# Optimization experiments

Hardware: AMD Instinct MI355X
Metric: run time of the kernel (lower is better)

Reference implementation:

```python
import jax, jax.numpy as jnp
import numpy as np

B, T = 2048, 512
H1, H2, H3 = 100, 60, 30


def _glorot(key, shape, fan):
    bound = 1.0 / np.sqrt(fan)
    return jax.random.uniform(key, shape, jnp.float32, -bound, bound)


def setup_inputs() -> dict:
    key = jax.random.key(0)
    ks = jax.random.split(key, 17)
    inp = {"x": jax.random.normal(ks[0], (B, T, 2), jnp.float32)}
    # layer 1: input 2 -> hidden 100
    inp["W_ih1"] = _glorot(ks[1], (H1, 2), H1)
    inp["W_hh1"] = _glorot(ks[2], (H1, H1), H1)
    inp["b_ih1"] = _glorot(ks[3], (H1,), H1)
    inp["b_hh1"] = _glorot(ks[4], (H1,), H1)
    # layer 2: 100 -> 60
    inp["W_ih2"] = _glorot(ks[5], (H2, H1), H2)
    inp["W_hh2"] = _glorot(ks[6], (H2, H2), H2)
    inp["b_ih2"] = _glorot(ks[7], (H2,), H2)
    inp["b_hh2"] = _glorot(ks[8], (H2,), H2)
    # layer 3: 60 -> 30
    inp["W_ih3"] = _glorot(ks[9], (H3, H2), H3)
    inp["W_hh3"] = _glorot(ks[10], (H3, H3), H3)
    inp["b_ih3"] = _glorot(ks[11], (H3,), H3)
    inp["b_hh3"] = _glorot(ks[12], (H3,), H3)
    # heads
    inp["W_o1"] = _glorot(ks[13], (10, H3), 10)
    inp["b_o1"] = _glorot(ks[14], (10,), 10)
    inp["W_o2"] = _glorot(ks[15], (2, 10), 2)
    inp["b_o2"] = _glorot(ks[16], (2,), 2)
    return inp


def rnn_layer(x, W_ih, W_hh, b_ih, b_hh):
    # x: [B, T, in]; precompute the time-parallel input projection once
    xp = jnp.einsum("bti,hi->bth", x, W_ih) + (b_ih + b_hh)  # [B, T, H]
    h0 = jnp.zeros((x.shape[0], W_hh.shape[0]), x.dtype)

    def step(h, xt):  # xt: [B, H]
        h = jnp.tanh(xt + h @ W_hh.T)
        return h, h

    _, ys = jax.lax.scan(step, h0, jnp.swapaxes(xp, 0, 1))  # [T, B, H]
    return jnp.swapaxes(ys, 0, 1)  # [B, T, H]


def reference(x, W_ih1, W_hh1, b_ih1, b_hh1, W_ih2, W_hh2, b_ih2, b_hh2,
              W_ih3, W_hh3, b_ih3, b_hh3, W_o1, b_o1, W_o2, b_o2):
    h = rnn_layer(x, W_ih1, W_hh1, b_ih1, b_hh1)
    h = rnn_layer(h, W_ih2, W_hh2, b_ih2, b_hh2)
    h = rnn_layer(h, W_ih3, W_hh3, b_ih3, b_hh3)
    o = jnp.einsum("bth,oh->bto", h, W_o1) + b_o1
    return jnp.einsum("bto,po->btp", o, W_o2) + b_o2  # [B, T, 2]
```

## Files before the change

### kernel.cpp

```cpp
#include <hip/hip_runtime.h>

typedef _Float16 v8hf __attribute__((ext_vector_type(8)));
typedef float    v4f  __attribute__((ext_vector_type(4)));

#define MFMA16(a, b, c) __builtin_amdgcn_mfma_f32_16x16x32_f16((a), (b), (c), 0, 0, 0)

#define TT 512
#define BT 16
#define NTH 1024

#define PBLK  8192u
#define H2OFF 4352u
#define H3OFF 6656u
#define XSTO  16384u
#define RINGO 49152u

__shared__ __align__(64) char SM[57344];

__device__ __forceinline__ v4f tanh4(v4f r) {
    const float KS = 2.8853900817779268f;
    const float CL = 13.8498724f;
    float z0 = __builtin_amdgcn_fmed3f(r[0] * KS, -CL, CL);
    float z1 = __builtin_amdgcn_fmed3f(r[1] * KS, -CL, CL);
    float z2 = __builtin_amdgcn_fmed3f(r[2] * KS, -CL, CL);
    float z3 = __builtin_amdgcn_fmed3f(r[3] * KS, -CL, CL);
    float a0 = __builtin_amdgcn_exp2f(z0) + 1.f;
    float a1 = __builtin_amdgcn_exp2f(z1) + 1.f;
    float a2 = __builtin_amdgcn_exp2f(z2) + 1.f;
    float a3 = __builtin_amdgcn_exp2f(z3) + 1.f;
    float P = a0 * a1, Q = a2 * a3;
    float R = __builtin_amdgcn_rcpf(P * Q);
    float iP = Q * R, iQ = P * R;
    v4f t;
    t[0] = 1.f - 2.f * (a1 * iP);
    t[1] = 1.f - 2.f * (a0 * iP);
    t[2] = 1.f - 2.f * (a3 * iQ);
    t[3] = 1.f - 2.f * (a2 * iQ);
    return t;
}

__global__ __launch_bounds__(NTH)
void rnn3_t16(const float* __restrict__ xg,
              const float* __restrict__ Wih1, const float* __restrict__ Whh1,
              const float* __restrict__ bih1, const float* __restrict__ bhh1,
              const float* __restrict__ Wih2, const float* __restrict__ Whh2,
              const float* __restrict__ bih2, const float* __restrict__ bhh2,
              const float* __restrict__ Wih3, const float* __restrict__ Whh3,
              const float* __restrict__ bih3, const float* __restrict__ bhh3,
              const float* __restrict__ Wo1,  const float* __restrict__ bo1,
              const float* __restrict__ Wo2,  const float* __restrict__ bo2,
              float* __restrict__ outg)
{
    const int tid   = threadIdx.x;
    const int lane  = tid & 63;
    const int wid   = tid >> 6;
    const int col   = lane & 15;
    const int g     = lane >> 4;
    const int bbase = blockIdx.x * BT;

    {
        float4 z = {0.f, 0.f, 0.f, 0.f};
        float4* p4 = (float4*)SM;
        for (int i = tid; i < 1024; i += NTH) p4[i] = z;
        for (int i = tid; i < BT * TT * 2; i += NTH) {
            float v = xg[(size_t)bbase * (TT * 2) + i];
            int b = i >> 10, r = i & 1023, t = r >> 1, c = r & 1;
            *(_Float16*)(SM + XSTO + (unsigned)t * 64u + (unsigned)b * 4u + (unsigned)c * 2u) = (_Float16)v;
        }
    }

    v8hf F[6];
    #pragma unroll
    for (int i = 0; i < 6; ++i) F[i] = (v8hf)(_Float16)0.f;
    float bb0 = 0.f;

    auto ldW = [&](const float* W, int rows, int cols, int j, int kt) -> v8hf {
        v8hf r;
        #pragma unroll
        for (int e = 0; e < 8; ++e) {
            const int k = kt * 32 + g * 8 + e;
            float v = (j < rows && k < cols) ? W[j * cols + k] : 0.f;
            r[e] = (_Float16)v;
        }
        return r;
    };
    auto ldW1 = [&](int j, int kt) -> v8hf {
        v8hf r;
        #pragma unroll
        for (int e = 0; e < 8; ++e) {
            const int k = kt * 32 + g * 8 + e;
            float v = 0.f;
            if (j < 100) {
                if (k < 100)       v = Whh1[j * 100 + k];
                else if (k == 112) v = Wih1[j * 2];
                else if (k == 113) v = Wih1[j * 2 + 1];
            }
            r[e] = (_Float16)v;
        }
        return r;
    };

    unsigned bRd = 0, bRd2 = 0, bRd3 = 0, bW1 = 0, bW2 = 0, bW3 = 0, bXw = 0, bRw = 0;
    unsigned xr = 0;

    if (wid < 7) {
        const int jA = 16 * wid + col;
        #pragma unroll
        for (int kt = 0; kt < 4; ++kt) F[kt] = ldW1(jA, kt);
        bb0 = (jA < 100) ? bih1[jA] + bhh1[jA] : 0.f;
        bRd = (unsigned)col * 272u + (unsigned)g * 16u;
        bW1 = (unsigned)(4 * g) * 272u + (unsigned)jA * 2u;
    } else if (wid == 7) {
        bXw = (unsigned)lane * 272u + 224u;
        xr  = XSTO + 64u + (unsigned)lane * 4u;
    } else if (wid < 12) {
        const int j2 = 16 * (wid - 8) + col;
        #pragma unroll
        for (int kt = 0; kt < 4; ++kt) F[kt] = ldW(Wih2, 60, 100, j2, kt);
        F[4] = ldW(Whh2, 60, 60, j2, 0);
        F[5] = ldW(Whh2, 60, 60, j2, 1);
        bb0 = (j2 < 60) ? bih2[j2] + bhh2[j2] : 0.f;
        bRd  = (unsigned)col * 272u + (unsigned)g * 16u;
        bRd2 = (unsigned)col * 144u + (unsigned)g * 16u;
        bW2  = (unsigned)(4 * g) * 144u + (unsigned)j2 * 2u;
    } else if (wid < 14) {
        const int j3 = 16 * (wid - 12) + col;
        F[0] = ldW(Wih3, 30, 60, j3, 0);
        F[1] = ldW(Wih3, 30, 60, j3, 1);
        F[2] = ldW(Whh3, 30, 30, j3, 0);
        bb0 = (j3 < 30) ? bih3[j3] + bhh3[j3] : 0.f;
        bRd2 = (unsigned)col * 144u + (unsigned)g * 16u;
        bRd3 = (unsigned)col * 80u + (unsigned)g * 16u;
        bW3  = (unsigned)(4 * g) * 80u + (unsigned)j3 * 2u;
    } else if (wid == 14) {
        #pragma unroll
        for (int e = 0; e < 8; ++e) {
            const int k = g * 8 + e;
            float v = 0.f;
            if (col < 2 && k < 30) {
                #pragma unroll
                for (int u = 0; u < 10; ++u) v += Wo2[col * 10 + u] * Wo1[u * 30 + k];
            }
            F[0][e] = (_Float16)v;
        }
        if (col < 2) {
            float bv = bo2[col];
            #pragma unroll
            for (int u = 0; u < 10; ++u) bv += Wo2[col * 10 + u] * bo1[u];
            bb0 = bv;
        }
        bRd3 = (unsigned)col * 80u + (unsigned)g * 16u;
        bRw  = RINGO + (unsigned)(4 * g) * 512u + (unsigned)col * 4u;
    }

    __syncthreads();
    if (tid < BT)
        *(unsigned*)(SM + (unsigned)tid * 272u + 224u) =
            *(const unsigned*)(SM + XSTO + (unsigned)tid * 4u);
    __syncthreads();

    auto flushfn = [&](int s) {
        const int tbase = s - 35;
        const unsigned rb = RINGO + (((unsigned)tbase & 63u) >> 1) * 16u;
        #pragma unroll
        for (int jj = 0; jj < 4; ++jj) {
            const int f = lane + 64 * jj;
            const int b = f >> 4, k = f & 15;
            float4 v = *(const float4*)(SM + rb + (unsigned)b * 512u + (unsigned)k * 16u);
            *(float4*)(outg + ((size_t)(bbase + b) * TT + tbase) * 2 + 4 * k) = v;
        }
    };

#define PHASE(RP, L1ON, L2ON, L3ON, HDON, XON, S) do {                                   \
    const unsigned RB_ = (RP) ? PBLK : 0u;                                               \
    const unsigned WB_ = (RP) ? 0u : PBLK;                                               \
    if (wid < 7) {                                                                       \
        if (L1ON) {                                                                      \
            v8hf A0 = *(const v8hf*)(SM + bRd + RB_ + 0u);                               \
            v8hf A1 = *(const v8hf*)(SM + bRd + RB_ + 64u);                              \
            v8hf A2 = *(const v8hf*)(SM + bRd + RB_ + 128u);                             \
            v8hf A3 = *(const v8hf*)(SM + bRd + RB_ + 192u);                             \
            v4f p = {bb0, bb0, bb0, bb0}, q = {0.f, 0.f, 0.f, 0.f};                      \
            p = MFMA16(A0, F[0], p); q = MFMA16(A1, F[1], q);                            \
            p = MFMA16(A2, F[2], p); q = MFMA16(A3, F[3], q);                            \
            v4f r = tanh4(p + q);                                                        \
            *(_Float16*)(SM + bW1 + WB_ + 0u)   = (_Float16)r[0];                        \
            *(_Float16*)(SM + bW1 + WB_ + 272u) = (_Float16)r[1];                        \
            *(_Float16*)(SM + bW1 + WB_ + 544u) = (_Float16)r[2];                        \
            *(_Float16*)(SM + bW1 + WB_ + 816u) = (_Float16)r[3];                        \
        }                                                                                \
    } else if (wid == 7) {                                                               \
        if (XON) {                                                                       \
            if (lane < 16) {                                                             \
                unsigned xv = *(const unsigned*)(SM + xr);                               \
                *(unsigned*)(SM + bXw + WB_) = xv;                                       \
            }                                                                            \
        }                                                                                \
        xr += 64u;                                                                       \
    } else if (wid < 12) {                                                               \
        if (L2ON) {                                                                      \
            v8hf A0 = *(const v8hf*)(SM + bRd + RB_ + 0u);                               \
            v8hf A1 = *(const v8hf*)(SM + bRd + RB_ + 64u);                              \
            v8hf A2 = *(const v8hf*)(SM + bRd + RB_ + 128u);                             \
            v8hf A3 = *(const v8hf*)(SM + bRd + RB_ + 192u);                             \
            v8hf B0 = *(const v8hf*)(SM + bRd2 + WB_ + H2OFF + 0u);                      \
            v8hf B1 = *(const v8hf*)(SM + bRd2 + WB_ + H2OFF + 64u);                     \
            v4f p = {bb0, bb0, bb0, bb0}, q = {0.f, 0.f, 0.f, 0.f};                      \
            p = MFMA16(A0, F[0], p); q = MFMA16(A1, F[1], q);                            \
            p = MFMA16(A2, F[2], p); q = MFMA16(A3, F[3], q);                            \
            p = MFMA16(B0, F[4], p); q = MFMA16(B1, F[5], q);                            \
            v4f r = tanh4(p + q);                                                        \
            *(_Float16*)(SM + bW2 + RB_ + H2OFF + 0u)   = (_Float16)r[0];                \
            *(_Float16*)(SM + bW2 + RB_ + H2OFF + 144u) = (_Float16)r[1];                \
            *(_Float16*)(SM + bW2 + RB_ + H2OFF + 288u) = (_Float16)r[2];                \
            *(_Float16*)(SM + bW2 + RB_ + H2OFF + 432u) = (_Float16)r[3];                \
        }                                                                                \
    } else if (wid < 14) {                                                               \
        if (L3ON) {                                                                      \
            v8hf B0 = *(const v8hf*)(SM + bRd2 + WB_ + H2OFF + 0u);                      \
            v8hf B1 = *(const v8hf*)(SM + bRd2 + WB_ + H2OFF + 64u);                     \
            v8hf C0 = *(const v8hf*)(SM + bRd3 + RB_ + H3OFF);                           \
            v4f p = {bb0, bb0, bb0, bb0}, q = {0.f, 0.f, 0.f, 0.f};                      \
            p = MFMA16(B0, F[0], p); q = MFMA16(B1, F[1], q);                            \
            p = MFMA16(C0, F[2], p);                                                     \
            v4f r = tanh4(p + q);                                                        \
            *(_Float16*)(SM + bW3 + WB_ + H3OFF + 0u)   = (_Float16)r[0];                \
            *(_Float16*)(SM + bW3 + WB_ + H3OFF + 80u)  = (_Float16)r[1];                \
            *(_Float16*)(SM + bW3 + WB_ + H3OFF + 160u) = (_Float16)r[2];                \
            *(_Float16*)(SM + bW3 + WB_ + H3OFF + 240u) = (_Float16)r[3];                \
        }                                                                                \
    } else if (wid == 14) {                                                              \
        if (HDON) {                                                                      \
            v8hf C0 = *(const v8hf*)(SM + bRd3 + RB_ + H3OFF);                           \
            v4f o = {bb0, bb0, bb0, bb0};                                                \
            o = MFMA16(C0, F[0], o);                                                     \
            const unsigned so = (((unsigned)(S) - 3u) & 63u) * 8u;                       \
            if (col < 2) {                                                               \
                *(float*)(SM + bRw + so + 0u)    = o[0];                                 \
                *(float*)(SM + bRw + so + 512u)  = o[1];                                 \
                *(float*)(SM + bRw + so + 1024u) = o[2];                                 \
                *(float*)(SM + bRw + so + 1536u) = o[3];                                 \
            }                                                                            \
        }                                                                                \
    } else {                                                                             \
        if ((S) >= 35 && (((S) - 4) & 31) == 31) flushfn((S));                           \
    }                                                                                    \
    __syncthreads();                                                                     \
} while (0)

    PHASE(0, 1, 0, 0, 0, 1, 0);
    PHASE(1, 1, 1, 0, 0, 1, 1);
    PHASE(0, 1, 1, 1, 0, 1, 2);
    PHASE(1, 1, 1, 1, 1, 1, 3);
    for (int s = 4; s < 510; s += 2) {
        PHASE(0, 1, 1, 1, 1, 1, s);
        PHASE(1, 1, 1, 1, 1, 1, s + 1);
    }
    PHASE(0, 1, 1, 1, 1, 1, 510);
    PHASE(1, 1, 1, 1, 1, 0, 511);
    PHASE(0, 0, 1, 1, 1, 0, 512);
    PHASE(1, 0, 0, 1, 1, 0, 513);
    PHASE(0, 0, 0, 0, 1, 0, 514);
    PHASE(1, 0, 0, 0, 0, 0, 515);
}

extern "C" void kernel_launch(void* const* d_in, const int* in_sizes, int n_in,
                              void* d_out, int out_size, void* d_ws, size_t ws_size,
                              hipStream_t stream) {
    (void)in_sizes; (void)n_in; (void)d_ws; (void)ws_size; (void)out_size;
    const float* x     = (const float*)d_in[0];
    const float* W_ih1 = (const float*)d_in[1];
    const float* W_hh1 = (const float*)d_in[2];
    const float* b_ih1 = (const float*)d_in[3];
    const float* b_hh1 = (const float*)d_in[4];
    const float* W_ih2 = (const float*)d_in[5];
    const float* W_hh2 = (const float*)d_in[6];
    const float* b_ih2 = (const float*)d_in[7];
    const float* b_hh2 = (const float*)d_in[8];
    const float* W_ih3 = (const float*)d_in[9];
    const float* W_hh3 = (const float*)d_in[10];
    const float* b_ih3 = (const float*)d_in[11];
    const float* b_hh3 = (const float*)d_in[12];
    const float* W_o1  = (const float*)d_in[13];
    const float* b_o1  = (const float*)d_in[14];
    const float* W_o2  = (const float*)d_in[15];
    const float* b_o2  = (const float*)d_in[16];
    float* out = (float*)d_out;

    rnn3_t16<<<2048 / BT, NTH, 0, stream>>>(
        x, W_ih1, W_hh1, b_ih1, b_hh1,
        W_ih2, W_hh2, b_ih2, b_hh2,
        W_ih3, W_hh3, b_ih3, b_hh3,
        W_o1, b_o1, W_o2, b_o2, out);
}
```

Measured before the change: 291.8 us.

## Halve block to 8 waves with double column tiles and register-prefetched inputs

Shrinks the block from 16 to 8 waves, so each wave computes two 16-column output tiles and the x-staging and flush duties are folded into compute waves. Layers 2, 3 and the head now prefetch their upstream hidden-state fragments into registers during the previous phase, which adds one pipeline stage of latency per layer. This removes the shared-memory load wait from the critical path after each barrier, at the cost of more register pressure. Layer-1 waves also get raised scheduling priority, and the prologue, epilogue and flush timing are stretched to match the deeper pipeline.

```diff
diff --git a/kernel.cpp b/kernel.cpp
--- a/kernel.cpp
+++ b/kernel.cpp
@@ -7,7 +7,7 @@
 
 #define TT 512
 #define BT 16
-#define NTH 1024
+#define NTH 512
 
 #define PBLK  8192u
 #define H2OFF 4352u
@@ -40,16 +40,16 @@
 }
 
 __global__ __launch_bounds__(NTH)
-void rnn3_t16(const float* __restrict__ xg,
-              const float* __restrict__ Wih1, const float* __restrict__ Whh1,
-              const float* __restrict__ bih1, const float* __restrict__ bhh1,
-              const float* __restrict__ Wih2, const float* __restrict__ Whh2,
-              const float* __restrict__ bih2, const float* __restrict__ bhh2,
-              const float* __restrict__ Wih3, const float* __restrict__ Whh3,
-              const float* __restrict__ bih3, const float* __restrict__ bhh3,
-              const float* __restrict__ Wo1,  const float* __restrict__ bo1,
-              const float* __restrict__ Wo2,  const float* __restrict__ bo2,
-              float* __restrict__ outg)
+void rnn3_pf(const float* __restrict__ xg,
+             const float* __restrict__ Wih1, const float* __restrict__ Whh1,
+             const float* __restrict__ bih1, const float* __restrict__ bhh1,
+             const float* __restrict__ Wih2, const float* __restrict__ Whh2,
+             const float* __restrict__ bih2, const float* __restrict__ bhh2,
+             const float* __restrict__ Wih3, const float* __restrict__ Whh3,
+             const float* __restrict__ bih3, const float* __restrict__ bhh3,
+             const float* __restrict__ Wo1,  const float* __restrict__ bo1,
+             const float* __restrict__ Wo2,  const float* __restrict__ bo2,
+             float* __restrict__ outg)
 {
     const int tid   = threadIdx.x;
     const int lane  = tid & 63;
@@ -69,10 +69,13 @@
         }
     }
 
-    v8hf F[6];
+    v8hf F[12];
     #pragma unroll
-    for (int i = 0; i < 6; ++i) F[i] = (v8hf)(_Float16)0.f;
-    float bb0 = 0.f;
+    for (int i = 0; i < 12; ++i) F[i] = (v8hf)(_Float16)0.f;
+    v8hf pf[2][4];
+    #pragma unroll
+    for (int i = 0; i < 4; ++i) { pf[0][i] = (v8hf)(_Float16)0.f; pf[1][i] = (v8hf)(_Float16)0.f; }
+    float bb0 = 0.f, bb1 = 0.f;
 
     auto ldW = [&](const float* W, int rows, int cols, int j, int kt) -> v8hf {
         v8hf r;
@@ -103,36 +106,46 @@
     unsigned bRd = 0, bRd2 = 0, bRd3 = 0, bW1 = 0, bW2 = 0, bW3 = 0, bXw = 0, bRw = 0;
     unsigned xr = 0;
 
-    if (wid < 7) {
-        const int jA = 16 * wid + col;
+    if (wid < 3) {
+        const int jA = 32 * wid + col;
+        #pragma unroll
+        for (int kt = 0; kt < 4; ++kt) { F[kt] = ldW1(jA, kt); F[4 + kt] = ldW1(jA + 16, kt); }
+        bb0 = (jA < 100) ? bih1[jA] + bhh1[jA] : 0.f;
+        bb1 = (jA + 16 < 100) ? bih1[jA + 16] + bhh1[jA + 16] : 0.f;
+        bRd = (unsigned)col * 272u + (unsigned)g * 16u;
+        bW1 = (unsigned)(4 * g) * 272u + (unsigned)jA * 2u;
+    } else if (wid == 3) {
+        const int jA = 96 + col;
         #pragma unroll
         for (int kt = 0; kt < 4; ++kt) F[kt] = ldW1(jA, kt);
         bb0 = (jA < 100) ? bih1[jA] + bhh1[jA] : 0.f;
         bRd = (unsigned)col * 272u + (unsigned)g * 16u;
         bW1 = (unsigned)(4 * g) * 272u + (unsigned)jA * 2u;
-    } else if (wid == 7) {
         bXw = (unsigned)lane * 272u + 224u;
         xr  = XSTO + 64u + (unsigned)lane * 4u;
-    } else if (wid < 12) {
-        const int j2 = 16 * (wid - 8) + col;
-        #pragma unroll
-        for (int kt = 0; kt < 4; ++kt) F[kt] = ldW(Wih2, 60, 100, j2, kt);
-        F[4] = ldW(Whh2, 60, 60, j2, 0);
-        F[5] = ldW(Whh2, 60, 60, j2, 1);
-        bb0 = (j2 < 60) ? bih2[j2] + bhh2[j2] : 0.f;
+    } else if (wid < 6) {
+        const int jA = 32 * (wid - 4) + col;
+        #pragma unroll
+        for (int kt = 0; kt < 4; ++kt) { F[kt] = ldW(Wih2, 60, 100, jA, kt); F[6 + kt] = ldW(Wih2, 60, 100, jA + 16, kt); }
+        F[4]  = ldW(Whh2, 60, 60, jA, 0);       F[5]  = ldW(Whh2, 60, 60, jA, 1);
+        F[10] = ldW(Whh2, 60, 60, jA + 16, 0);  F[11] = ldW(Whh2, 60, 60, jA + 16, 1);
+        bb0 = (jA < 60) ? bih2[jA] + bhh2[jA] : 0.f;
+        bb1 = (jA + 16 < 60) ? bih2[jA + 16] + bhh2[jA + 16] : 0.f;
         bRd  = (unsigned)col * 272u + (unsigned)g * 16u;
         bRd2 = (unsigned)col * 144u + (unsigned)g * 16u;
-        bW2  = (unsigned)(4 * g) * 144u + (unsigned)j2 * 2u;
-    } else if (wid < 14) {
-        const int j3 = 16 * (wid - 12) + col;
-        F[0] = ldW(Wih3, 30, 60, j3, 0);
-        F[1] = ldW(Wih3, 30, 60, j3, 1);
-        F[2] = ldW(Whh3, 30, 30, j3, 0);
-        bb0 = (j3 < 30) ? bih3[j3] + bhh3[j3] : 0.f;
+        bW2  = (unsigned)(4 * g) * 144u + (unsigned)jA * 2u;
+    } else if (wid == 6) {
+        const int jA = col;
+        F[0] = ldW(Wih3, 30, 60, jA, 0);       F[1] = ldW(Wih3, 30, 60, jA, 1);
+        F[2] = ldW(Whh3, 30, 30, jA, 0);
+        F[3] = ldW(Wih3, 30, 60, jA + 16, 0);  F[4] = ldW(Wih3, 30, 60, jA + 16, 1);
+        F[5] = ldW(Whh3, 30, 30, jA + 16, 0);
+        bb0 = (jA < 30) ? bih3[jA] + bhh3[jA] : 0.f;
+        bb1 = (jA + 16 < 30) ? bih3[jA + 16] + bhh3[jA + 16] : 0.f;
         bRd2 = (unsigned)col * 144u + (unsigned)g * 16u;
         bRd3 = (unsigned)col * 80u + (unsigned)g * 16u;
-        bW3  = (unsigned)(4 * g) * 80u + (unsigned)j3 * 2u;
-    } else if (wid == 14) {
+        bW3  = (unsigned)(4 * g) * 80u + (unsigned)jA * 2u;
+    } else {
         #pragma unroll
         for (int e = 0; e < 8; ++e) {
             const int k = g * 8 + e;
@@ -159,8 +172,10 @@
             *(const unsigned*)(SM + XSTO + (unsigned)tid * 4u);
     __syncthreads();
 
+    if (wid < 4) __builtin_amdgcn_s_setprio(1);
+
     auto flushfn = [&](int s) {
-        const int tbase = s - 35;
+        const int tbase = s - 39;
         const unsigned rb = RINGO + (((unsigned)tbase & 63u) >> 1) * 16u;
         #pragma unroll
         for (int jj = 0; jj < 4; ++jj) {
@@ -174,7 +189,37 @@
 #define PHASE(RP, L1ON, L2ON, L3ON, HDON, XON, S) do {                                   \
     const unsigned RB_ = (RP) ? PBLK : 0u;                                               \
     const unsigned WB_ = (RP) ? 0u : PBLK;                                               \
-    if (wid < 7) {                                                                       \
+    if (wid < 3) {                                                                       \
+        if (L1ON) {                                                                      \
+            v8hf A0 = *(const v8hf*)(SM + bRd + RB_ + 0u);                               \
+            v8hf A1 = *(const v8hf*)(SM + bRd + RB_ + 64u);                              \
+            v8hf A2 = *(const v8hf*)(SM + bRd + RB_ + 128u);                             \
+            v8hf A3 = *(const v8hf*)(SM + bRd + RB_ + 192u);                             \
+            { v4f p = {bb0, bb0, bb0, bb0}, q = {0.f, 0.f, 0.f, 0.f};                    \
+              p = MFMA16(A0, F[0], p); q = MFMA16(A1, F[1], q);                          \
+              p = MFMA16(A2, F[2], p); q = MFMA16(A3, F[3], q);                          \
+              v4f r = tanh4(p + q);                                                      \
+              *(_Float16*)(SM + bW1 + WB_ + 0u)   = (_Float16)r[0];                      \
+              *(_Float16*)(SM + bW1 + WB_ + 272u) = (_Float16)r[1];                      \
+              *(_Float16*)(SM + bW1 + WB_ + 544u) = (_Float16)r[2];                      \
+              *(_Float16*)(SM + bW1 + WB_ + 816u) = (_Float16)r[3]; }                    \
+            { v4f p = {bb1, bb1, bb1, bb1}, q = {0.f, 0.f, 0.f, 0.f};                    \
+              p = MFMA16(A0, F[4], p); q = MFMA16(A1, F[5], q);                          \
+              p = MFMA16(A2, F[6], p); q = MFMA16(A3, F[7], q);                          \
+              v4f r = tanh4(p + q);                                                      \
+              *(_Float16*)(SM + bW1 + WB_ + 32u)  = (_Float16)r[0];                      \
+              *(_Float16*)(SM + bW1 + WB_ + 304u) = (_Float16)r[1];                      \
+              *(_Float16*)(SM + bW1 + WB_ + 576u) = (_Float16)r[2];                      \
+              *(_Float16*)(SM + bW1 + WB_ + 848u) = (_Float16)r[3]; }                    \
+        }                                                                                \
+    } else if (wid == 3) {                                                               \
+        if (XON) {                                                                       \
+            if (lane < 16) {                                                             \
+                unsigned xv = *(const unsigned*)(SM + xr);                               \
+                *(unsigned*)(SM + bXw + WB_) = xv;                                       \
+            }                                                                            \
+        }                                                                                \
+        xr += 64u;                                                                       \
         if (L1ON) {                                                                      \
             v8hf A0 = *(const v8hf*)(SM + bRd + RB_ + 0u);                               \
             v8hf A1 = *(const v8hf*)(SM + bRd + RB_ + 64u);                              \
@@ -189,52 +234,60 @@
             *(_Float16*)(SM + bW1 + WB_ + 544u) = (_Float16)r[2];                        \
             *(_Float16*)(SM + bW1 + WB_ + 816u) = (_Float16)r[3];                        \
         }                                                                                \
-    } else if (wid == 7) {                                                               \
-        if (XON) {                                                                       \
-            if (lane < 16) {                                                             \
-                unsigned xv = *(const unsigned*)(SM + xr);                               \
-                *(unsigned*)(SM + bXw + WB_) = xv;                                       \
-            }                                                                            \
-        }                                                                                \
-        xr += 64u;                                                                       \
-    } else if (wid < 12) {                                                               \
+    } else if (wid < 6) {                                                                \
         if (L2ON) {                                                                      \
-            v8hf A0 = *(const v8hf*)(SM + bRd + RB_ + 0u);                               \
-            v8hf A1 = *(const v8hf*)(SM + bRd + RB_ + 64u);                              \
-            v8hf A2 = *(const v8hf*)(SM + bRd + RB_ + 128u);                             \
-            v8hf A3 = *(const v8hf*)(SM + bRd + RB_ + 192u);                             \
-            v8hf B0 = *(const v8hf*)(SM + bRd2 + WB_ + H2OFF + 0u);                      \
-            v8hf B1 = *(const v8hf*)(SM + bRd2 + WB_ + H2OFF + 64u);                     \
-            v4f p = {bb0, bb0, bb0, bb0}, q = {0.f, 0.f, 0.f, 0.f};                      \
-            p = MFMA16(A0, F[0], p); q = MFMA16(A1, F[1], q);                            \
-            p = MFMA16(A2, F[2], p); q = MFMA16(A3, F[3], q);                            \
-            p = MFMA16(B0, F[4], p); q = MFMA16(B1, F[5], q);                            \
-            v4f r = tanh4(p + q);                                                        \
-            *(_Float16*)(SM + bW2 + RB_ + H2OFF + 0u)   = (_Float16)r[0];                \
-            *(_Float16*)(SM + bW2 + RB_ + H2OFF + 144u) = (_Float16)r[1];                \
-            *(_Float16*)(SM + bW2 + RB_ + H2OFF + 288u) = (_Float16)r[2];                \
-            *(_Float16*)(SM + bW2 + RB_ + H2OFF + 432u) = (_Float16)r[3];                \
-        }                                                                                \
-    } else if (wid < 14) {                                                               \
+            v8hf B0 = *(const v8hf*)(SM + bRd2 + RB_ + H2OFF + 0u);                      \
+            v8hf B1 = *(const v8hf*)(SM + bRd2 + RB_ + H2OFF + 64u);                     \
+            { v4f p = {bb0, bb0, bb0, bb0}, q = {0.f, 0.f, 0.f, 0.f};                    \
+              p = MFMA16(pf[RP][0], F[0], p); q = MFMA16(pf[RP][1], F[1], q);            \
+              p = MFMA16(pf[RP][2], F[2], p); q = MFMA16(pf[RP][3], F[3], q);            \
+              p = MFMA16(B0, F[4], p);        q = MFMA16(B1, F[5], q);                   \
+              v4f r = tanh4(p + q);                                                      \
+              *(_Float16*)(SM + bW2 + WB_ + H2OFF + 0u)   = (_Float16)r[0];              \
+              *(_Float16*)(SM + bW2 + WB_ + H2OFF + 144u) = (_Float16)r[1];              \
+              *(_Float16*)(SM + bW2 + WB_ + H2OFF + 288u) = (_Float16)r[2];              \
+              *(_Float16*)(SM + bW2 + WB_ + H2OFF + 432u) = (_Float16)r[3]; }            \
+            { v4f p = {bb1, bb1, bb1, bb1}, q = {0.f, 0.f, 0.f, 0.f};                    \
+              p = MFMA16(pf[RP][0], F[6], p); q = MFMA16(pf[RP][1], F[7], q);            \
+              p = MFMA16(pf[RP][2], F[8], p); q = MFMA16(pf[RP][3], F[9], q);            \
+              p = MFMA16(B0, F[10], p);       q = MFMA16(B1, F[11], q);                  \
+              v4f r = tanh4(p + q);                                                      \
+              *(_Float16*)(SM + bW2 + WB_ + H2OFF + 32u)  = (_Float16)r[0];              \
+              *(_Float16*)(SM + bW2 + WB_ + H2OFF + 176u) = (_Float16)r[1];              \
+              *(_Float16*)(SM + bW2 + WB_ + H2OFF + 320u) = (_Float16)r[2];              \
+              *(_Float16*)(SM + bW2 + WB_ + H2OFF + 464u) = (_Float16)r[3]; }            \
+        }                                                                                \
+        pf[(RP) ^ 1][0] = *(const v8hf*)(SM + bRd + RB_ + 0u);                           \
+        pf[(RP) ^ 1][1] = *(const v8hf*)(SM + bRd + RB_ + 64u);                          \
+        pf[(RP) ^ 1][2] = *(const v8hf*)(SM + bRd + RB_ + 128u);                         \
+        pf[(RP) ^ 1][3] = *(const v8hf*)(SM + bRd + RB_ + 192u);                         \
+    } else if (wid == 6) {                                                               \
         if (L3ON) {                                                                      \
-            v8hf B0 = *(const v8hf*)(SM + bRd2 + WB_ + H2OFF + 0u);                      \
-            v8hf B1 = *(const v8hf*)(SM + bRd2 + WB_ + H2OFF + 64u);                     \
             v8hf C0 = *(const v8hf*)(SM + bRd3 + RB_ + H3OFF);                           \
-            v4f p = {bb0, bb0, bb0, bb0}, q = {0.f, 0.f, 0.f, 0.f};                      \
-            p = MFMA16(B0, F[0], p); q = MFMA16(B1, F[1], q);                            \
-            p = MFMA16(C0, F[2], p);                                                     \
-            v4f r = tanh4(p + q);                                                        \
-            *(_Float16*)(SM + bW3 + WB_ + H3OFF + 0u)   = (_Float16)r[0];                \
-            *(_Float16*)(SM + bW3 + WB_ + H3OFF + 80u)  = (_Float16)r[1];                \
-            *(_Float16*)(SM + bW3 + WB_ + H3OFF + 160u) = (_Float16)r[2];                \
-            *(_Float16*)(SM + bW3 + WB_ + H3OFF + 240u) = (_Float16)r[3];                \
-        }                                                                                \
-    } else if (wid == 14) {                                                              \
+            { v4f p = {bb0, bb0, bb0, bb0}, q = {0.f, 0.f, 0.f, 0.f};                    \
+              p = MFMA16(pf[RP][0], F[0], p); q = MFMA16(pf[RP][1], F[1], q);            \
+              p = MFMA16(C0, F[2], p);                                                   \
+              v4f r = tanh4(p + q);                                                      \
+              *(_Float16*)(SM + bW3 + WB_ + H3OFF + 0u)   = (_Float16)r[0];              \
+              *(_Float16*)(SM + bW3 + WB_ + H3OFF + 80u)  = (_Float16)r[1];              \
+              *(_Float16*)(SM + bW3 + WB_ + H3OFF + 160u) = (_Float16)r[2];              \
+              *(_Float16*)(SM + bW3 + WB_ + H3OFF + 240u) = (_Float16)r[3]; }            \
+            { v4f p = {bb1, bb1, bb1, bb1}, q = {0.f, 0.f, 0.f, 0.f};                    \
+              p = MFMA16(pf[RP][0], F[3], p); q = MFMA16(pf[RP][1], F[4], q);            \
+              p = MFMA16(C0, F[5], p);                                                   \
+              v4f r = tanh4(p + q);                                                      \
+              *(_Float16*)(SM + bW3 + WB_ + H3OFF + 32u)  = (_Float16)r[0];              \
+              *(_Float16*)(SM + bW3 + WB_ + H3OFF + 112u) = (_Float16)r[1];              \
+              *(_Float16*)(SM + bW3 + WB_ + H3OFF + 192u) = (_Float16)r[2];              \
+              *(_Float16*)(SM + bW3 + WB_ + H3OFF + 272u) = (_Float16)r[3]; }            \
+        }                                                                                \
+        pf[(RP) ^ 1][0] = *(const v8hf*)(SM + bRd2 + RB_ + H2OFF + 0u);                  \
+        pf[(RP) ^ 1][1] = *(const v8hf*)(SM + bRd2 + RB_ + H2OFF + 64u);                 \
+    } else {                                                                             \
         if (HDON) {                                                                      \
-            v8hf C0 = *(const v8hf*)(SM + bRd3 + RB_ + H3OFF);                           \
             v4f o = {bb0, bb0, bb0, bb0};                                                \
-            o = MFMA16(C0, F[0], o);                                                     \
-            const unsigned so = (((unsigned)(S) - 3u) & 63u) * 8u;                       \
+            o = MFMA16(pf[RP][0], F[0], o);                                              \
+            const unsigned so = (((unsigned)(S) - 6u) & 63u) * 8u;                       \
             if (col < 2) {                                                               \
                 *(float*)(SM + bRw + so + 0u)    = o[0];                                 \
                 *(float*)(SM + bRw + so + 512u)  = o[1];                                 \
@@ -242,26 +295,32 @@
                 *(float*)(SM + bRw + so + 1536u) = o[3];                                 \
             }                                                                            \
         }                                                                                \
-    } else {                                                                             \
-        if ((S) >= 35 && (((S) - 4) & 31) == 31) flushfn((S));                           \
+        pf[(RP) ^ 1][0] = *(const v8hf*)(SM + bRd3 + RB_ + H3OFF);                       \
+        if ((S) >= 39 && (((S) - 39) & 31) == 0) flushfn((S));                           \
     }                                                                                    \
     __syncthreads();                                                                     \
 } while (0)
 
     PHASE(0, 1, 0, 0, 0, 1, 0);
-    PHASE(1, 1, 1, 0, 0, 1, 1);
-    PHASE(0, 1, 1, 1, 0, 1, 2);
-    PHASE(1, 1, 1, 1, 1, 1, 3);
-    for (int s = 4; s < 510; s += 2) {
+    PHASE(1, 1, 0, 0, 0, 1, 1);
+    PHASE(0, 1, 1, 0, 0, 1, 2);
+    PHASE(1, 1, 1, 0, 0, 1, 3);
+    PHASE(0, 1, 1, 1, 0, 1, 4);
+    PHASE(1, 1, 1, 1, 0, 1, 5);
+    for (int s = 6; s < 510; s += 2) {
         PHASE(0, 1, 1, 1, 1, 1, s);
         PHASE(1, 1, 1, 1, 1, 1, s + 1);
     }
     PHASE(0, 1, 1, 1, 1, 1, 510);
     PHASE(1, 1, 1, 1, 1, 0, 511);
     PHASE(0, 0, 1, 1, 1, 0, 512);
-    PHASE(1, 0, 0, 1, 1, 0, 513);
-    PHASE(0, 0, 0, 0, 1, 0, 514);
-    PHASE(1, 0, 0, 0, 0, 0, 515);
+    PHASE(1, 0, 1, 1, 1, 0, 513);
+    PHASE(0, 0, 0, 1, 1, 0, 514);
+    PHASE(1, 0, 0, 1, 1, 0, 515);
+    PHASE(0, 0, 0, 0, 1, 0, 516);
+    PHASE(1, 0, 0, 0, 1, 0, 517);
+    PHASE(0, 0, 0, 0, 0, 0, 518);
+    PHASE(1, 0, 0, 0, 0, 0, 519);
 }
 
 extern "C" void kernel_launch(void* const* d_in, const int* in_sizes, int n_in,
@@ -287,7 +346,7 @@
     const float* b_o2  = (const float*)d_in[16];
     float* out = (float*)d_out;
 
-    rnn3_t16<<<2048 / BT, NTH, 0, stream>>>(
+    rnn3_pf<<<2048 / BT, NTH, 0, stream>>>(
         x, W_ih1, W_hh1, b_ih1, b_hh1,
         W_ih2, W_hh2, b_ih2, b_hh2,
         W_ih3, W_hh3, b_ih3, b_hh3,
```

After: 306.0 us. 1.05x slower.
